# Kernel optimization log

Measured on AMD Instinct MI355X. Metric: run time of the kernel, lower is better.

The kernel has to match this reference:

```python
import jax, jax.numpy as jnp
import numpy as np

B, N, E, F, D = 8, 2000, 64000, 1024, 128
NEG_SLOPE = 0.01  # torch LeakyReLU default

def leaky(x):
    return jnp.where(x >= 0, x, NEG_SLOPE * x)

def gcn_conv(x, ei, W, b):
    # PyG GCNConv: add self loops, symmetric norm, x @ W, scatter-sum, + bias
    src, tgt = ei[0], ei[1]
    loops = jnp.arange(N, dtype=src.dtype)
    src_a = jnp.concatenate([src, loops])
    tgt_a = jnp.concatenate([tgt, loops])
    deg = jax.ops.segment_sum(jnp.ones(src_a.shape, x.dtype), tgt_a, num_segments=N)
    dinv = jnp.where(deg > 0, jax.lax.rsqrt(deg), 0.0)
    norm = dinv[src_a] * dinv[tgt_a]  # [E+N]
    h = x @ W                          # [N, F]
    out = jax.ops.segment_sum(norm[:, None] * h[src_a], tgt_a, num_segments=N)
    return out + b

gcn_conv_b = jax.vmap(gcn_conv, in_axes=(0, 0, None, None))

def setup_inputs() -> dict:
    key = jax.random.key(0)
    ks = jax.random.split(key, 16)
    s = lambda fan: 1.0 / np.sqrt(fan)
    return {
        "x1": jax.random.normal(ks[0], (B, N, F), jnp.float32),
        "ei1": jax.random.randint(ks[1], (B, 2, E), 0, N, jnp.int32),
        "x2": jax.random.normal(ks[2], (B, N, F), jnp.float32),
        "ei2": jax.random.randint(ks[3], (B, 2, E), 0, N, jnp.int32),
        "Wg1": jax.random.normal(ks[4], (F, F), jnp.float32) * s(F),
        "bg1": jnp.zeros((F,), jnp.float32),
        "Wf1": jax.random.normal(ks[5], (F, D), jnp.float32) * s(F),
        "bf1": jnp.zeros((D,), jnp.float32),
        "Wg2": jax.random.normal(ks[6], (F, F), jnp.float32) * s(F),
        "bg2": jnp.zeros((F,), jnp.float32),
        "Wf2": jax.random.normal(ks[7], (F, D), jnp.float32) * s(F),
        "bf2": jnp.zeros((D,), jnp.float32),
        "W1": jax.random.normal(ks[8], (2 * D, 256), jnp.float32) * s(2 * D),
        "b1": jnp.zeros((256,), jnp.float32),
        "W2": jax.random.normal(ks[9], (256, 64), jnp.float32) * s(256),
        "b2": jnp.zeros((64,), jnp.float32),
        "Wo": jax.random.normal(ks[10], (64, 1), jnp.float32) * s(64),
        "bo": jnp.zeros((1,), jnp.float32),
    }

def reference(x1, ei1, x2, ei2, Wg1, bg1, Wf1, bf1, Wg2, bg2, Wf2, bf2,
              W1, b1, W2, b2, Wo, bo):
    # branch 1
    h1 = leaky(gcn_conv_b(x1, ei1, Wg1, bg1))       # [B, N, F]
    g1 = jnp.mean(h1, axis=1)                        # [B, F]
    g1 = leaky(g1 @ Wf1 + bf1)                       # [B, D] (dropout = eval identity)
    # branch 2
    h2 = leaky(gcn_conv_b(x2, ei2, Wg2, bg2))
    g2 = jnp.mean(h2, axis=1)
    g2 = leaky(g2 @ Wf2 + bf2)
    # head
    xc = jnp.concatenate([g1, g2], axis=1)           # [B, 2D]
    xc = leaky(xc @ W1 + b1)
    xc = leaky(xc @ W2 + b2)
    return jax.nn.sigmoid(xc @ Wo + bo)              # [B, 1]
```

## Files before the change

kernel.cpp:

```cpp
#include <hip/hip_runtime.h>
#include <stdint.h>

#define B 8
#define NN 2000
#define EG 64000
#define FF 1024
#define DD 128
#define NCHUNK 125
#define CG 5

#define NB_CONV 32000
#define NB_WT   2048
#define NB_DEG  4000
#define NTK 16
#define NB_G8 504

typedef short short8 __attribute__((ext_vector_type(8)));
typedef float f32x4 __attribute__((ext_vector_type(4)));
typedef float f32x2 __attribute__((ext_vector_type(2)));

__device__ __forceinline__ unsigned short f2bf(float f) {
    union { float f; unsigned int u; } v; v.f = f;
    unsigned int u = v.u;
    unsigned int r = u + 0x7FFFu + ((u >> 16) & 1u);
    return (unsigned short)(r >> 16);
}
__device__ __forceinline__ float leaky(float v) { return v >= 0.0f ? v : 0.01f * v; }

__device__ __forceinline__ void acc8p(f32x2* __restrict__ r, float w, uint4 v) {
    union { unsigned int u; float f; } c;
    f32x2 wv = {w, w};
    f32x2 h;
    c.u = v.x << 16;          h.x = c.f;
    c.u = v.x & 0xffff0000u;  h.y = c.f;
    r[0] += wv * h;
    c.u = v.y << 16;          h.x = c.f;
    c.u = v.y & 0xffff0000u;  h.y = c.f;
    r[1] += wv * h;
    c.u = v.z << 16;          h.x = c.f;
    c.u = v.z & 0xffff0000u;  h.y = c.f;
    r[2] += wv * h;
    c.u = v.w << 16;          h.x = c.f;
    c.u = v.w & 0xffff0000u;  h.y = c.f;
    r[3] += wv * h;
}

__global__ void k_prep(const float* __restrict__ x_a, const float* __restrict__ x_b,
                       unsigned short* __restrict__ xb,
                       const float* __restrict__ Wg_a, const float* __restrict__ Wg_b,
                       unsigned short* __restrict__ wT,
                       const int* __restrict__ ei_a, const int* __restrict__ ei_b,
                       int* __restrict__ degi) {
    int blk = blockIdx.x;
    int tid = threadIdx.x;
    __shared__ float tile[32][33];
    if (blk < NB_CONV) {
        int i = blk * 256 + tid;
        float4 v = (i < NB_CONV * 128) ? ((const float4*)x_a)[i]
                                       : ((const float4*)x_b)[i - NB_CONV * 128];
        ushort4 o;
        o.x = f2bf(v.x); o.y = f2bf(v.y); o.z = f2bf(v.z); o.w = f2bf(v.w);
        ((ushort4*)xb)[i] = o;
    } else if (blk < NB_CONV + NB_WT) {
        int b2 = blk - NB_CONV;
        int z = b2 >> 10, rem = b2 & 1023;
        int by = rem >> 5, bx = rem & 31;
        int tx = tid & 31, ty = tid >> 5;
        int k0 = by * 32, n0 = bx * 32;
        const float* Wg = z ? Wg_b : Wg_a;
        unsigned short* o = wT + (size_t)z * FF * FF;
#pragma unroll
        for (int r = 0; r < 4; ++r) {
            int row = ty + r * 8;
            tile[row][tx] = Wg[(k0 + row) * FF + n0 + tx];
        }
        __syncthreads();
#pragma unroll
        for (int r = 0; r < 4; ++r) {
            int row = ty + r * 8;
            o[(n0 + row) * FF + k0 + tx] = f2bf(tile[tx][row]);
        }
    } else {
        int i = (blk - NB_CONV - NB_WT) * 256 + tid;
        int g = i / EG, e = i - g * EG;
        const int* ei = (g < B) ? (ei_a + (size_t)g * 2 * EG)
                                : (ei_b + (size_t)(g - B) * 2 * EG);
        int t = ei[EG + e];
        atomicAdd(&degi[g * NN + t], 1);
    }
}

__global__ void k_scan(const int* __restrict__ degi, int* __restrict__ csr_off,
                       int* __restrict__ cursor, float* __restrict__ dinv) {
    int g = blockIdx.x, t = threadIdx.x;
    __shared__ int part[256];
    int loc[8];
    int s = 0;
#pragma unroll
    for (int i = 0; i < 8; ++i) {
        int n = t * 8 + i;
        int c = (n < NN) ? degi[g * NN + n] : 0;
        if (n < NN) dinv[g * NN + n] = rsqrtf((float)(c + 1));
        loc[i] = s;
        s += c;
    }
    part[t] = s;
    __syncthreads();
    for (int off = 1; off < 256; off <<= 1) {
        int v = (t >= off) ? part[t - off] : 0;
        __syncthreads();
        part[t] += v;
        __syncthreads();
    }
    int base = part[t] - s;
#pragma unroll
    for (int i = 0; i < 8; ++i) {
        int n = t * 8 + i;
        if (n < NN) {
            int o = base + loc[i];
            csr_off[g * (NN + 1) + n] = o;
            cursor[g * NN + n] = o;
        }
    }
    if (t == 255) csr_off[g * (NN + 1) + NN] = part[255];
}

__launch_bounds__(512, 2) __global__
void k_gemm8(const unsigned short* __restrict__ Abf, const unsigned short* __restrict__ wT,
             unsigned short* __restrict__ Hbf,
             const int* __restrict__ ei_a, const int* __restrict__ ei_b,
             int* __restrict__ cursor, const float* __restrict__ dinv,
             int2* __restrict__ epk) {
    __shared__ __align__(16) char smem[131072];
    int bid = blockIdx.x;
    int wg = (bid & 7) * 63 + (bid >> 3);
    int mt = wg >> 2, nt = wg & 3;
    int set = (mt >= 63) ? 1 : 0;
    int m0 = set * 16000 + (mt - set * 63) * 256;
    int n0 = nt * 256;
    int mlim = set * 16000 + 16000;
    const unsigned short* Bg = wT + (size_t)set * FF * FF;

    int tid = threadIdx.x;
    int lane = tid & 63, wave = tid >> 6;
    int wr = wave >> 2, wc = wave & 3;
    int l15 = lane & 15, q = lane >> 4;
    int arow = wr * 128 + l15;
    int brow = wc * 64 + l15;
    int sw = l15 & 7;
    unsigned so0 = (unsigned)((q ^ sw) << 4);
    unsigned so1 = (unsigned)(((4 + q) ^ sw) << 4);
    int srow = tid >> 3;
    int col8s = (tid & 7) ^ (srow & 7);
    unsigned wbase = (unsigned)wave << 10;

    f32x4 acc[8][4];
#pragma unroll
    for (int i = 0; i < 8; ++i)
#pragma unroll
        for (int j = 0; j < 4; ++j) acc[i][j] = (f32x4){0.f, 0.f, 0.f, 0.f};

    auto stage = [&](int ktn, int isB, int h) {
        const unsigned short* gsrc = isB ? Bg : Abf;
        int x0 = isB ? n0 : m0;
        int r1 = x0 + h * 64 + srow;
        int kb = ktn * 64 + col8s * 8;
        unsigned db = ((unsigned)(ktn & 1) << 16) | ((unsigned)isB << 15)
                    | ((unsigned)h << 13) | wbase;
        __builtin_amdgcn_global_load_lds(
            (const __attribute__((address_space(1))) unsigned int*)(gsrc + (size_t)r1 * FF + kb),
            (__attribute__((address_space(3))) unsigned int*)&smem[db], 16, 0, 0);
        __builtin_amdgcn_global_load_lds(
            (const __attribute__((address_space(1))) unsigned int*)(gsrc + (size_t)(r1 + 128) * FF + kb),
            (__attribute__((address_space(3))) unsigned int*)&smem[db + 16384], 16, 0, 0);
    };

    stage(0, 1, 0); stage(0, 1, 1); stage(0, 0, 0); stage(0, 0, 1);
    asm volatile("s_waitcnt vmcnt(2)" ::: "memory");
    __builtin_amdgcn_s_barrier();

    unsigned bb = 0;
    auto lda = [&](int i, unsigned so) -> short8 {
        return *(const short8*)&smem[bb + ((unsigned)(arow + i * 16) << 7) + so];
    };
    auto ldb = [&](int j, unsigned so) -> short8 {
        return *(const short8*)&smem[bb + 32768u + ((unsigned)(brow + j * 16) << 7) + so];
    };

#pragma unroll 1
    for (int kt = 0; kt < NTK; ++kt) {
        bb = (unsigned)(kt & 1) << 16;
        short8 fa[4], fb[4];
#pragma unroll
        for (int j = 0; j < 4; ++j) fb[j] = ldb(j, so0);
#pragma unroll
        for (int i = 0; i < 4; ++i) fa[i] = lda(i, so0);
        stage(kt + 1, 1, 0);
        __builtin_amdgcn_s_barrier();
        asm volatile("s_waitcnt lgkmcnt(0)" ::: "memory");
        __builtin_amdgcn_sched_barrier(0);
        __builtin_amdgcn_s_setprio(1);
#pragma unroll
        for (int i = 0; i < 4; ++i)
#pragma unroll
            for (int j = 0; j < 4; ++j)
                acc[i][j] = __builtin_amdgcn_mfma_f32_16x16x32_bf16(fa[i], fb[j], acc[i][j], 0, 0, 0);
        __builtin_amdgcn_s_setprio(0);
        asm volatile("s_waitcnt vmcnt(2)" ::: "memory");
        __builtin_amdgcn_s_barrier();
#pragma unroll
        for (int i = 0; i < 4; ++i) fa[i] = lda(i + 4, so0);
        stage(kt + 1, 1, 1);
        __builtin_amdgcn_s_barrier();
        asm volatile("s_waitcnt lgkmcnt(0)" ::: "memory");
        __builtin_amdgcn_sched_barrier(0);
        __builtin_amdgcn_s_setprio(1);
#pragma unroll
        for (int i = 0; i < 4; ++i)
#pragma unroll
            for (int j = 0; j < 4; ++j)
                acc[i + 4][j] = __builtin_amdgcn_mfma_f32_16x16x32_bf16(fa[i], fb[j], acc[i + 4][j], 0, 0, 0);
        __builtin_amdgcn_s_setprio(0);
        __builtin_amdgcn_s_barrier();
#pragma unroll
        for (int j = 0; j < 4; ++j) fb[j] = ldb(j, so1);
#pragma unroll
        for (int i = 0; i < 4; ++i) fa[i] = lda(i, so1);
        stage(kt + 1, 0, 0);
        __builtin_amdgcn_s_barrier();
        asm volatile("s_waitcnt lgkmcnt(0)" ::: "memory");
        __builtin_amdgcn_sched_barrier(0);
        __builtin_amdgcn_s_setprio(1);
#pragma unroll
        for (int i = 0; i < 4; ++i)
#pragma unroll
            for (int j = 0; j < 4; ++j)
                acc[i][j] = __builtin_amdgcn_mfma_f32_16x16x32_bf16(fa[i], fb[j], acc[i][j], 0, 0, 0);
        __builtin_amdgcn_s_setprio(0);
        __builtin_amdgcn_s_barrier();
#pragma unroll
        for (int i = 0; i < 4; ++i) fa[i] = lda(i + 4, so1);
        stage(kt + 1, 0, 1);
        __builtin_amdgcn_s_barrier();
        asm volatile("s_waitcnt lgkmcnt(0)" ::: "memory");
        __builtin_amdgcn_sched_barrier(0);
        __builtin_amdgcn_s_setprio(1);
#pragma unroll
        for (int i = 0; i < 4; ++i)
#pragma unroll
            for (int j = 0; j < 4; ++j)
                acc[i + 4][j] = __builtin_amdgcn_mfma_f32_16x16x32_bf16(fa[i], fb[j], acc[i + 4][j], 0, 0, 0);
        __builtin_amdgcn_s_setprio(0);
        asm volatile("s_waitcnt vmcnt(2)" ::: "memory");
        __builtin_amdgcn_s_barrier();
    }

#pragma unroll
    for (int i = 0; i < 8; ++i) {
#pragma unroll
        for (int j = 0; j < 4; ++j) {
            int n = n0 + wc * 64 + j * 16 + l15;
#pragma unroll
            for (int v = 0; v < 4; ++v) {
                int m = m0 + wr * 128 + i * 16 + q * 4 + v;
                if (m < mlim) Hbf[(size_t)m * FF + n] = f2bf(acc[i][j][v]);
            }
        }
    }

    int ebase = bid * 512 + tid;
#pragma unroll
    for (int r = 0; r < 4; ++r) {
        int idx = ebase + r * (NB_G8 * 512);
        if (idx < 16 * EG) {
            int gg = idx / EG, e = idx - gg * EG;
            const int* ei = (gg < B) ? (ei_a + (size_t)gg * 2 * EG)
                                     : (ei_b + (size_t)(gg - B) * 2 * EG);
            int s = ei[e];
            int t = ei[EG + e];
            int pos = atomicAdd(&cursor[gg * NN + t], 1);
            int2 p;
            p.x = s;
            p.y = __float_as_int(dinv[gg * NN + s] * dinv[gg * NN + t]);
            epk[(size_t)gg * EG + pos] = p;
        }
    }
}

__launch_bounds__(256) __global__
void k_aggreduce(const unsigned short* __restrict__ Hbf, const int* __restrict__ csr_off,
                 const int2* __restrict__ epk, const float* __restrict__ dinv,
                 const float* __restrict__ bg_a, const float* __restrict__ bg_b,
                 float* __restrict__ part) {
    int blk = blockIdx.x;
    int phase = blk / 1000;
    int bp = blk - phase * 1000;
    int half = phase & 1;
    int g = (phase >> 1) * 8 + (bp & 7);
    int chunk = bp >> 3;
    int tid = threadIdx.x;
    int team = tid >> 6;
    int lane = tid & 63;
    int f0 = half * 512 + lane * 8;
    int n0 = chunk * 16 + team * 4;
    const unsigned short* Hb = Hbf + (size_t)g * NN * FF;
    const int2* ep = epk + (size_t)g * EG;
    const float* bg = (g < B) ? bg_a : bg_b;

    f32x2 bgv[4];
#pragma unroll
    for (int i = 0; i < 4; ++i) bgv[i] = (f32x2){bg[f0 + 2 * i], bg[f0 + 2 * i + 1]};
    f32x2 bsum[4];
#pragma unroll
    for (int i = 0; i < 4; ++i) bsum[i] = (f32x2){0.f, 0.f};

    for (int nn = 0; nn < 4; ++nn) {
        int n = n0 + nn;
        float dn = dinv[g * NN + n];
        int beg = csr_off[g * (NN + 1) + n];
        int end = csr_off[g * (NN + 1) + n + 1];
        f32x2 racc[4];
#pragma unroll
        for (int i = 0; i < 4; ++i) racc[i] = (f32x2){0.f, 0.f};
        {
            uint4 sv = *(const uint4*)&Hb[(n << 10) + f0];
            acc8p(racc, dn * dn, sv);
        }
        int j = beg;
        int2 pe0, pe1, pe2, pe3;
        if (j + 4 <= end) { pe0 = ep[j]; pe1 = ep[j + 1]; pe2 = ep[j + 2]; pe3 = ep[j + 3]; }
        for (; j + 8 <= end; j += 4) {
            int2 e0 = pe0, e1 = pe1, e2 = pe2, e3 = pe3;
            pe0 = ep[j + 4]; pe1 = ep[j + 5]; pe2 = ep[j + 6]; pe3 = ep[j + 7];
            uint4 v0 = *(const uint4*)&Hb[(e0.x << 10) + f0];
            uint4 v1 = *(const uint4*)&Hb[(e1.x << 10) + f0];
            uint4 v2 = *(const uint4*)&Hb[(e2.x << 10) + f0];
            uint4 v3 = *(const uint4*)&Hb[(e3.x << 10) + f0];
            acc8p(racc, __int_as_float(e0.y), v0);
            acc8p(racc, __int_as_float(e1.y), v1);
            acc8p(racc, __int_as_float(e2.y), v2);
            acc8p(racc, __int_as_float(e3.y), v3);
        }
        if (j + 4 <= end) {
            uint4 v0 = *(const uint4*)&Hb[(pe0.x << 10) + f0];
            uint4 v1 = *(const uint4*)&Hb[(pe1.x << 10) + f0];
            uint4 v2 = *(const uint4*)&Hb[(pe2.x << 10) + f0];
            uint4 v3 = *(const uint4*)&Hb[(pe3.x << 10) + f0];
            acc8p(racc, __int_as_float(pe0.y), v0);
            acc8p(racc, __int_as_float(pe1.y), v1);
            acc8p(racc, __int_as_float(pe2.y), v2);
            acc8p(racc, __int_as_float(pe3.y), v3);
            j += 4;
        }
        for (; j < end; ++j) {
            int2 e = ep[j];
            uint4 v = *(const uint4*)&Hb[(e.x << 10) + f0];
            acc8p(racc, __int_as_float(e.y), v);
        }
#pragma unroll
        for (int i = 0; i < 4; ++i) {
            f32x2 t = racc[i] + bgv[i];
            bsum[i].x += leaky(t.x);
            bsum[i].y += leaky(t.y);
        }
    }

    __shared__ float red[3][64 * 9];
    if (team > 0) {
#pragma unroll
        for (int i = 0; i < 4; ++i) {
            red[team - 1][lane * 9 + 2 * i]     = bsum[i].x;
            red[team - 1][lane * 9 + 2 * i + 1] = bsum[i].y;
        }
    }
    __syncthreads();
    if (team == 0) {
        float* o = part + ((size_t)g * NCHUNK + chunk) * FF + f0;
        float r[8];
#pragma unroll
        for (int i = 0; i < 4; ++i) {
            r[2 * i]     = bsum[i].x;
            r[2 * i + 1] = bsum[i].y;
        }
#pragma unroll
        for (int t = 0; t < 3; ++t)
#pragma unroll
            for (int i = 0; i < 8; ++i) r[i] += red[t][lane * 9 + i];
        float4 a = {r[0], r[1], r[2], r[3]};
        float4 c = {r[4], r[5], r[6], r[7]};
        *(float4*)&o[0] = a;
        *(float4*)&o[4] = c;
    }
}

__global__ void k_gsum1(const float* __restrict__ part, float* __restrict__ part2) {
    int blk = blockIdx.x;
    int g = blk / 20;
    int rem = blk - g * 20;
    int fq = rem / CG, cg = rem - fq * CG;
    int f = fq * 256 + threadIdx.x;
    const float* p = part + (size_t)g * NCHUNK * FF + (size_t)cg * 25 * FF + f;
    float s = 0.f;
#pragma unroll 5
    for (int c = 0; c < 25; ++c) s += p[(size_t)c * FF];
    part2[((size_t)g * CG + cg) * FF + f] = s;
}

__launch_bounds__(512) __global__
void k_fc(const float* __restrict__ part2, const float* __restrict__ Wf_a,
          const float* __restrict__ bf_a, const float* __restrict__ Wf_b,
          const float* __restrict__ bf_b, float* __restrict__ g12) {
    int g = blockIdx.x, t = threadIdx.x;
    int d = t & 127, slice = t >> 7;
    __shared__ float gs[FF];
    __shared__ float red[4][DD];
    const float* p = part2 + (size_t)g * CG * FF;
#pragma unroll
    for (int i = 0; i < 2; ++i) {
        int f = i * 512 + t;
        float s = 0.f;
#pragma unroll
        for (int c = 0; c < CG; ++c) s += p[(size_t)c * FF + f];
        gs[f] = s;
    }
    __syncthreads();
    const float* Wf = (g < B) ? Wf_a : Wf_b;
    const float* bfv = (g < B) ? bf_a : bf_b;
    float acc = 0.f;
    int fbase = slice * 256;
#pragma unroll 8
    for (int ff = 0; ff < 256; ++ff) {
        int f = fbase + ff;
        acc += gs[f] * Wf[f * DD + d];
    }
    red[slice][d] = acc;
    __syncthreads();
    if (t < DD) {
        float a = red[0][t] + red[1][t] + red[2][t] + red[3][t];
        a = a * (1.0f / (float)NN) + bfv[t];
        g12[g * DD + t] = leaky(a);
    }
}

__launch_bounds__(256) __global__
void k_head(const float* __restrict__ g, const float* __restrict__ W1, const float* __restrict__ b1,
            const float* __restrict__ W2, const float* __restrict__ b2,
            const float* __restrict__ Wo, const float* __restrict__ bo, float* __restrict__ out) {
    __shared__ float xc[8][256];
    __shared__ float l1[8][256];
    __shared__ float l2[8][64];
    int t = threadIdx.x;
#pragma unroll
    for (int i = 0; i < 8; ++i) {
        int idx = i * 256 + t;
        int b = idx >> 8, j = idx & 255;
        xc[b][j] = (j < DD) ? g[b * DD + j] : g[B * DD + b * DD + (j - DD)];
    }
    __syncthreads();
    {
        int j = t;
        float a[8];
#pragma unroll
        for (int b = 0; b < 8; ++b) a[b] = b1[j];
        for (int k = 0; k < 256; ++k) {
            float w = W1[k * 256 + j];
#pragma unroll
            for (int b = 0; b < 8; ++b) a[b] += xc[b][k] * w;
        }
#pragma unroll
        for (int b = 0; b < 8; ++b) l1[b][j] = leaky(a[b]);
    }
    __syncthreads();
    if (t < 64) {
        int j = t;
        float a[8];
#pragma unroll
        for (int b = 0; b < 8; ++b) a[b] = b2[j];
        for (int k = 0; k < 256; ++k) {
            float w = W2[k * 64 + j];
#pragma unroll
            for (int b = 0; b < 8; ++b) a[b] += l1[b][k] * w;
        }
#pragma unroll
        for (int b = 0; b < 8; ++b) l2[b][j] = leaky(a[b]);
    }
    __syncthreads();
    if (t < 8) {
        float a = bo[0];
        for (int k = 0; k < 64; ++k) a += l2[t][k] * Wo[k];
        out[t] = 1.0f / (1.0f + expf(-a));
    }
}

extern "C" void kernel_launch(void* const* d_in, const int* in_sizes, int n_in,
                              void* d_out, int out_size, void* d_ws, size_t ws_size,
                              hipStream_t stream) {
    const float* x1  = (const float*)d_in[0];
    const int*   ei1 = (const int*)d_in[1];
    const float* x2  = (const float*)d_in[2];
    const int*   ei2 = (const int*)d_in[3];
    const float* Wg1 = (const float*)d_in[4];
    const float* bg1 = (const float*)d_in[5];
    const float* Wf1 = (const float*)d_in[6];
    const float* bf1 = (const float*)d_in[7];
    const float* Wg2 = (const float*)d_in[8];
    const float* bg2 = (const float*)d_in[9];
    const float* Wf2 = (const float*)d_in[10];
    const float* bf2 = (const float*)d_in[11];
    const float* W1  = (const float*)d_in[12];
    const float* b1  = (const float*)d_in[13];
    const float* W2  = (const float*)d_in[14];
    const float* b2  = (const float*)d_in[15];
    const float* Wo  = (const float*)d_in[16];
    const float* bo  = (const float*)d_in[17];
    float* out = (float*)d_out;

    auto align = [](size_t v) { return (v + 255) & ~(size_t)255; };
    size_t need = 0;
    size_t o_deg  = need; need += align((size_t)16 * NN * 4);
    size_t o_dinv = need; need += align((size_t)16 * NN * 4);
    size_t o_csr  = need; need += align((size_t)16 * (NN + 1) * 4);
    size_t o_cur  = need; need += align((size_t)16 * NN * 4);
    size_t o_epk  = need; need += align((size_t)16 * EG * 8);
    size_t o_xbf  = need; need += align(((size_t)16 * NN + 128) * FF * 2);
    size_t o_wT   = need; need += align((size_t)2 * FF * FF * 2);
    size_t o_hbf  = need; need += align((size_t)16 * NN * FF * 2);
    size_t o_part = need; need += align((size_t)16 * NCHUNK * FF * 4);
    size_t o_pt2  = need; need += align((size_t)16 * CG * FF * 4);
    size_t o_g12  = need; need += align((size_t)16 * DD * 4);
    (void)need;

    char* w = (char*)d_ws;
    int* degi    = (int*)(w + o_deg);
    float* dinv  = (float*)(w + o_dinv);
    int* csr     = (int*)(w + o_csr);
    int* cur     = (int*)(w + o_cur);
    int2* epk    = (int2*)(w + o_epk);
    unsigned short* xbf = (unsigned short*)(w + o_xbf);
    unsigned short* wT  = (unsigned short*)(w + o_wT);
    unsigned short* hbf = (unsigned short*)(w + o_hbf);
    float* part  = (float*)(w + o_part);
    float* part2 = (float*)(w + o_pt2);
    float* g12   = (float*)(w + o_g12);

    hipMemsetAsync(degi, 0, (size_t)16 * NN * 4, stream);
    k_prep<<<NB_CONV + NB_WT + NB_DEG, 256, 0, stream>>>(x1, x2, xbf, Wg1, Wg2, wT,
                                                         ei1, ei2, degi);
    k_scan<<<16, 256, 0, stream>>>(degi, csr, cur, dinv);
    k_gemm8<<<NB_G8, 512, 0, stream>>>(xbf, wT, hbf, ei1, ei2, cur, dinv, epk);
    k_aggreduce<<<4000, 256, 0, stream>>>(hbf, csr, epk, dinv, bg1, bg2, part);
    k_gsum1<<<16 * 20, 256, 0, stream>>>(part, part2);
    k_fc<<<16, 512, 0, stream>>>(part2, Wf1, bf1, Wf2, bf2, g12);
    k_head<<<1, 256, 0, stream>>>(g12, W1, b1, W2, b2, Wo, bo, out);
}
```

Baseline: 546.6 us.

## Re-layout GEMM LDS tiles as k-chunk-major and prefetch deeper across k-halves

Replaces the XOR-swizzled row-major LDS tile layout with a k-chunk-major layout, where each 16-byte column chunk of 64 (or 256) rows is stored contiguously. Fragment reads become simple strided addresses. The global-to-LDS staging is reorganised by k-half instead of row-half, so the next tile's second half and the tile after's first half are loaded while the current tile is consumed, and the vmcnt waits are relaxed accordingly. The goal is fewer LDS bank conflicts, less address arithmetic, and deeper load/compute overlap. In exchange it adds more in-flight loads, clamps redundant loads past the last tile, and makes correctness depend on the buffer reuse ordering.

Measured after the change: 559.1 us. 2.3% more time.

```diff
diff --git a/kernel.cpp b/kernel.cpp
--- a/kernel.cpp
+++ b/kernel.cpp
@@ -147,12 +147,8 @@
     int l15 = lane & 15, q = lane >> 4;
     int arow = wr * 128 + l15;
     int brow = wc * 64 + l15;
-    int sw = l15 & 7;
-    unsigned so0 = (unsigned)((q ^ sw) << 4);
-    unsigned so1 = (unsigned)(((4 + q) ^ sw) << 4);
-    int srow = tid >> 3;
-    int col8s = (tid & 7) ^ (srow & 7);
-    unsigned wbase = (unsigned)wave << 10;
+    unsigned aoff = (unsigned)(q * 4096 + arow * 16);
+    unsigned boff = 32768u + (unsigned)(q * 4096 + brow * 16);
 
     f32x4 acc[8][4];
 #pragma unroll
@@ -160,42 +156,39 @@
 #pragma unroll
         for (int j = 0; j < 4; ++j) acc[i][j] = (f32x4){0.f, 0.f, 0.f, 0.f};
 
-    auto stage = [&](int ktn, int isB, int h) {
+    auto stage = [&](int ktn, int isB, int h, int buf) {
+        int kcl = (ktn < NTK) ? ktn : NTK - 1;
         const unsigned short* gsrc = isB ? Bg : Abf;
         int x0 = isB ? n0 : m0;
-        int r1 = x0 + h * 64 + srow;
-        int kb = ktn * 64 + col8s * 8;
-        unsigned db = ((unsigned)(ktn & 1) << 16) | ((unsigned)isB << 15)
-                    | ((unsigned)h << 13) | wbase;
-        __builtin_amdgcn_global_load_lds(
-            (const __attribute__((address_space(1))) unsigned int*)(gsrc + (size_t)r1 * FF + kb),
-            (__attribute__((address_space(3))) unsigned int*)&smem[db], 16, 0, 0);
-        __builtin_amdgcn_global_load_lds(
-            (const __attribute__((address_space(1))) unsigned int*)(gsrc + (size_t)(r1 + 128) * FF + kb),
-            (__attribute__((address_space(3))) unsigned int*)&smem[db + 16384], 16, 0, 0);
+        int kc = kcl * 64 + h * 32;
+#pragma unroll
+        for (int l = 0; l < 2; ++l) {
+            int s = wave * 2 + l;
+            int c = s & 3, rb = s >> 2;
+            unsigned db = ((unsigned)buf << 16) | ((unsigned)isB << 15) | ((unsigned)h << 14)
+                        | ((unsigned)c << 12) | ((unsigned)rb << 10);
+            __builtin_amdgcn_global_load_lds(
+                (const __attribute__((address_space(1))) unsigned int*)
+                    (gsrc + (size_t)(x0 + rb * 64 + lane) * FF + kc + c * 8),
+                (__attribute__((address_space(3))) unsigned int*)&smem[db], 16, 0, 0);
+        }
     };
 
-    stage(0, 1, 0); stage(0, 1, 1); stage(0, 0, 0); stage(0, 0, 1);
-    asm volatile("s_waitcnt vmcnt(2)" ::: "memory");
+    stage(0, 0, 0, 0); stage(0, 1, 0, 0); stage(0, 0, 1, 0); stage(0, 1, 1, 0);
+    stage(1, 0, 0, 1); stage(1, 1, 0, 1);
+    asm volatile("s_waitcnt vmcnt(4)" ::: "memory");
     __builtin_amdgcn_s_barrier();
-
-    unsigned bb = 0;
-    auto lda = [&](int i, unsigned so) -> short8 {
-        return *(const short8*)&smem[bb + ((unsigned)(arow + i * 16) << 7) + so];
-    };
-    auto ldb = [&](int j, unsigned so) -> short8 {
-        return *(const short8*)&smem[bb + 32768u + ((unsigned)(brow + j * 16) << 7) + so];
-    };
 
 #pragma unroll 1
     for (int kt = 0; kt < NTK; ++kt) {
-        bb = (unsigned)(kt & 1) << 16;
+        int buf = kt & 1, nbuf = buf ^ 1;
+        unsigned bb = (unsigned)buf << 16;
         short8 fa[4], fb[4];
 #pragma unroll
-        for (int j = 0; j < 4; ++j) fb[j] = ldb(j, so0);
-#pragma unroll
-        for (int i = 0; i < 4; ++i) fa[i] = lda(i, so0);
-        stage(kt + 1, 1, 0);
+        for (int j = 0; j < 4; ++j) fb[j] = *(const short8*)&smem[bb + boff + (unsigned)(j << 8)];
+#pragma unroll
+        for (int i = 0; i < 4; ++i) fa[i] = *(const short8*)&smem[bb + aoff + (unsigned)(i << 8)];
+        stage(kt + 1, 0, 1, nbuf);
         __builtin_amdgcn_s_barrier();
         asm volatile("s_waitcnt lgkmcnt(0)" ::: "memory");
         __builtin_amdgcn_sched_barrier(0);
@@ -206,11 +199,10 @@
             for (int j = 0; j < 4; ++j)
                 acc[i][j] = __builtin_amdgcn_mfma_f32_16x16x32_bf16(fa[i], fb[j], acc[i][j], 0, 0, 0);
         __builtin_amdgcn_s_setprio(0);
-        asm volatile("s_waitcnt vmcnt(2)" ::: "memory");
-        __builtin_amdgcn_s_barrier();
-#pragma unroll
-        for (int i = 0; i < 4; ++i) fa[i] = lda(i + 4, so0);
-        stage(kt + 1, 1, 1);
+        __builtin_amdgcn_s_barrier();
+#pragma unroll
+        for (int i = 0; i < 4; ++i) fa[i] = *(const short8*)&smem[bb + aoff + (unsigned)((i + 4) << 8)];
+        stage(kt + 1, 1, 1, nbuf);
         __builtin_amdgcn_s_barrier();
         asm volatile("s_waitcnt lgkmcnt(0)" ::: "memory");
         __builtin_amdgcn_sched_barrier(0);
@@ -223,10 +215,10 @@
         __builtin_amdgcn_s_setprio(0);
         __builtin_amdgcn_s_barrier();
 #pragma unroll
-        for (int j = 0; j < 4; ++j) fb[j] = ldb(j, so1);
-#pragma unroll
-        for (int i = 0; i < 4; ++i) fa[i] = lda(i, so1);
-        stage(kt + 1, 0, 0);
+        for (int j = 0; j < 4; ++j) fb[j] = *(const short8*)&smem[bb + boff + 16384u + (unsigned)(j << 8)];
+#pragma unroll
+        for (int i = 0; i < 4; ++i) fa[i] = *(const short8*)&smem[bb + aoff + 16384u + (unsigned)(i << 8)];
+        stage(kt + 2, 0, 0, buf);
         __builtin_amdgcn_s_barrier();
         asm volatile("s_waitcnt lgkmcnt(0)" ::: "memory");
         __builtin_amdgcn_sched_barrier(0);
@@ -239,8 +231,8 @@
         __builtin_amdgcn_s_setprio(0);
         __builtin_amdgcn_s_barrier();
 #pragma unroll
-        for (int i = 0; i < 4; ++i) fa[i] = lda(i + 4, so1);
-        stage(kt + 1, 0, 1);
+        for (int i = 0; i < 4; ++i) fa[i] = *(const short8*)&smem[bb + aoff + 16384u + (unsigned)((i + 4) << 8)];
+        stage(kt + 2, 1, 0, buf);
         __builtin_amdgcn_s_barrier();
         asm volatile("s_waitcnt lgkmcnt(0)" ::: "memory");
         __builtin_amdgcn_sched_barrier(0);
@@ -251,7 +243,7 @@
             for (int j = 0; j < 4; ++j)
                 acc[i + 4][j] = __builtin_amdgcn_mfma_f32_16x16x32_bf16(fa[i], fb[j], acc[i + 4][j], 0, 0, 0);
         __builtin_amdgcn_s_setprio(0);
-        asm volatile("s_waitcnt vmcnt(2)" ::: "memory");
+        asm volatile("s_waitcnt vmcnt(4)" ::: "memory");
         __builtin_amdgcn_s_barrier();
     }
 
```
